# Performance work log

Hardware: AMD Instinct MI355X
Metric: run time of the kernel (lower is better)

## Reference

```python
import jax, jax.numpy as jnp
import numpy as np

N_NODES = 100000
N_EDGES = 1600000
N_GRAPHS = 64


def setup_inputs() -> dict:
    key = jax.random.key(0)
    ks = jax.random.split(key, 12)
    x = jax.random.normal(ks[0], (N_NODES, 3), dtype=jnp.float32)
    edge_index = jax.random.randint(ks[1], (2, N_EDGES), 0, N_NODES)
    edge_attr = jax.random.uniform(ks[2], (N_EDGES,), dtype=jnp.float32)
    batch = jnp.sort(jax.random.randint(ks[3], (N_NODES,), 0, N_GRAPHS))

    def glorot(k, shape):
        lim = float(np.sqrt(6.0 / (shape[0] + shape[1])))
        return jax.random.uniform(k, shape, jnp.float32, -lim, lim)

    W1 = glorot(ks[4], (3, 100));    b1 = jnp.zeros((100,), jnp.float32)
    W2 = glorot(ks[5], (100, 200));  b2 = jnp.zeros((200,), jnp.float32)
    Wl1 = glorot(ks[6], (200, 100)); bl1 = jnp.zeros((100,), jnp.float32)
    Wl2 = glorot(ks[7], (100, 1));   bl2 = jnp.zeros((1,), jnp.float32)
    return {"x": x, "edge_attr": edge_attr, "W1": W1, "b1": b1, "W2": W2,
            "b2": b2, "Wl1": Wl1, "bl1": bl1, "Wl2": Wl2, "bl2": bl2,
            "edge_index": edge_index, "batch": batch}


def gcn_conv(x, edge_index, edge_weight, W, b):
    # PyG GCNConv: linear transform, add self-loops (weight 1), symmetric
    # deg^{-1/2} normalization, scatter-add messages source->target, + bias.
    h = x @ W                                   # [N, out]
    n = h.shape[0]
    loops = jnp.arange(n)
    row = jnp.concatenate([edge_index[0], loops])   # sources
    col = jnp.concatenate([edge_index[1], loops])   # targets
    w = jnp.concatenate([edge_weight, jnp.ones((n,), edge_weight.dtype)])
    deg = jax.ops.segment_sum(w, col, num_segments=n)
    dinv = jnp.where(deg > 0, jax.lax.rsqrt(deg), jnp.zeros_like(deg))
    norm = dinv[row] * w * dinv[col]                # [E+N]
    out = jax.ops.segment_sum(norm[:, None] * h[row], col, num_segments=n)
    return out + b


def reference(x, edge_attr, W1, b1, W2, b2, Wl1, bl1, Wl2, bl2, edge_index, batch):
    h = jax.nn.silu(gcn_conv(x, edge_index, edge_attr, W1, b1))
    h = jax.nn.silu(gcn_conv(h, edge_index, edge_attr, W2, b2))
    # global_mean_pool over graphs in the batch
    sums = jax.ops.segment_sum(h, batch, num_segments=N_GRAPHS)
    counts = jax.ops.segment_sum(jnp.ones((h.shape[0],), h.dtype), batch,
                                 num_segments=N_GRAPHS)
    pooled = sums / jnp.maximum(counts, 1.0)[:, None]   # [G, 200]
    h = jax.nn.silu(pooled @ Wl1 + bl1)
    out = h @ Wl2 + bl2                                  # [G, 1]
    return out.squeeze()
```

## Files before the change

### kernel.cpp

```cpp
#include <hip/hip_runtime.h>

#define NN 100000
#define NE 1600000
#define NG 64
#define CAP 64
#define NPB 80
#define NBUCK 391
#define NBLK 391
#define EPB 4096

__device__ __forceinline__ float silu_f(float x) { return x / (1.0f + __expf(-x)); }

__global__ void k_hist(const int* __restrict__ col, int* __restrict__ hist,
                       float* __restrict__ pooled2) {
  __shared__ int h[NBUCK];
  int tid = threadIdx.x;
  for (int i = tid; i < NBUCK; i += 256) h[i] = 0;
  for (int i = blockIdx.x * 256 + tid; i < NG * 64 * 200; i += NBLK * 256)
    pooled2[i] = 0.0f;
  __syncthreads();
  int s = blockIdx.x * EPB;
  for (int i = 0; i < EPB / 1024; ++i) {
    int e = s + i * 1024 + tid * 4;
    if (e + 3 < NE) {
      int4 c4 = *(const int4*)(col + e);
      atomicAdd(&h[c4.x >> 8], 1);
      atomicAdd(&h[c4.y >> 8], 1);
      atomicAdd(&h[c4.z >> 8], 1);
      atomicAdd(&h[c4.w >> 8], 1);
    } else {
      for (int j = 0; j < 4; ++j) {
        int ee = e + j;
        if (ee < NE) atomicAdd(&h[col[ee] >> 8], 1);
      }
    }
  }
  __syncthreads();
  for (int i = tid; i < NBUCK; i += 256)
    hist[blockIdx.x * NBUCK + i] = h[i];
}

__global__ void k_bscan(const int* __restrict__ hist, int* __restrict__ off_bb,
                        int* __restrict__ tot) {
  __shared__ int m[NBLK][16];
  int tid = threadIdx.x;
  int b0 = blockIdx.x * 16;
  int cb = tid & 15, rr = tid >> 4;
  for (int r = rr; r < NBLK; r += 16) {
    int b = b0 + cb;
    m[r][cb] = (b < NBUCK) ? hist[r * NBUCK + b] : 0;
  }
  __syncthreads();
  if (tid < 16) {
    int run = 0;
    for (int r = 0; r < NBLK; ++r) { int v = m[r][tid]; m[r][tid] = run; run += v; }
    if (b0 + tid < NBUCK) tot[b0 + tid] = run;
  }
  __syncthreads();
  for (int r = rr; r < NBLK; r += 16) {
    int b = b0 + cb;
    if (b < NBUCK) off_bb[r * NBUCK + b] = m[r][cb];
  }
}

__global__ void k_scatter(const int* __restrict__ row, const int* __restrict__ col,
                          const float* __restrict__ ew, const int* __restrict__ off_bb,
                          const int* __restrict__ tot, int* __restrict__ gbase,
                          int2* __restrict__ sorted) {
  __shared__ int pos[NBUCK];
  __shared__ int bs[NBUCK];
  int tid = threadIdx.x;
  if (tid < 64) {
    int lane = tid;
    int loc[7];
    int ssum = 0;
    for (int i = 0; i < 7; ++i) {
      int b = lane * 7 + i;
      loc[i] = ssum;
      ssum += (b < NBUCK) ? tot[b] : 0;
    }
    int inc = ssum;
    for (int d = 1; d < 64; d <<= 1) {
      int t = __shfl_up(inc, d, 64);
      if (lane >= d) inc += t;
    }
    int excl = inc - ssum;
    for (int i = 0; i < 7; ++i) {
      int b = lane * 7 + i;
      if (b < NBUCK) bs[b] = excl + loc[i];
    }
  }
  __syncthreads();
  for (int i = tid; i < NBUCK; i += 256)
    pos[i] = off_bb[blockIdx.x * NBUCK + i] + bs[i];
  if (blockIdx.x == 0) {
    for (int i = tid; i < NBUCK; i += 256) gbase[i] = bs[i];
    if (tid == 0) gbase[NBUCK] = NE;
  }
  __syncthreads();
  int s = blockIdx.x * EPB;
  for (int i = 0; i < EPB / 1024; ++i) {
    int e = s + i * 1024 + tid * 4;
    if (e + 3 < NE) {
      int4 r4 = *(const int4*)(row + e);
      int4 c4 = *(const int4*)(col + e);
      float4 w4 = *(const float4*)(ew + e);
      int p0 = atomicAdd(&pos[c4.x >> 8], 1);
      int p1 = atomicAdd(&pos[c4.y >> 8], 1);
      int p2 = atomicAdd(&pos[c4.z >> 8], 1);
      int p3 = atomicAdd(&pos[c4.w >> 8], 1);
      sorted[p0] = make_int2(r4.x | ((c4.x & 255) << 17), __float_as_int(w4.x));
      sorted[p1] = make_int2(r4.y | ((c4.y & 255) << 17), __float_as_int(w4.y));
      sorted[p2] = make_int2(r4.z | ((c4.z & 255) << 17), __float_as_int(w4.z));
      sorted[p3] = make_int2(r4.w | ((c4.w & 255) << 17), __float_as_int(w4.w));
    } else {
      for (int j = 0; j < 4; ++j) {
        int ee = e + j;
        if (ee < NE) {
          int c = col[ee];
          int p = atomicAdd(&pos[c >> 8], 1);
          sorted[p] = make_int2(row[ee] | ((c & 255) << 17), __float_as_int(ew[ee]));
        }
      }
    }
  }
}

__global__ void k_group(const int* __restrict__ gbase, const int2* __restrict__ sorted,
                        int* __restrict__ cur, int2* __restrict__ buck,
                        float* __restrict__ dinv, const float* __restrict__ x,
                        float* __restrict__ y) {
  __shared__ int cnt[256];
  __shared__ float wsum[256];
  int b = blockIdx.x, tid = threadIdx.x;
  int s = gbase[b], e = gbase[b + 1];
  cnt[tid] = 0; wsum[tid] = 0.0f;
  __syncthreads();
  for (int i = s + tid; i < e; i += 256) {
    int2 pk = sorted[i];
    int node = (pk.x >> 17) & 255;
    int rank = atomicAdd(&cnt[node], 1);
    atomicAdd(&wsum[node], __int_as_float(pk.y));
    if (rank < CAP)
      buck[(((size_t)b * 256 + node) << 6) + rank] = make_int2(pk.x & 0x1FFFF, pk.y);
  }
  __syncthreads();
  int gnode = b * 256 + tid;
  if (gnode < NN) {
    cur[gnode] = cnt[tid];
    float di = rsqrtf(wsum[tid] + 1.0f);
    dinv[gnode] = di;
    y[3 * gnode + 0] = di * x[3 * gnode + 0];
    y[3 * gnode + 1] = di * x[3 * gnode + 1];
    y[3 * gnode + 2] = di * x[3 * gnode + 2];
  }
}

__global__ void k_agg1z(const int* __restrict__ cur, const int2* __restrict__ buck,
                        const float* __restrict__ dinv, const float* __restrict__ y,
                        const float* __restrict__ W1, const float* __restrict__ b1,
                        float* __restrict__ z1p) {
  int wave = threadIdx.x >> 6, lane = threadIdx.x & 63;
  int sub = lane >> 4, rank = lane & 15;
  int cbase = blockIdx.x * 16 + wave * 4;
  int c = cbase + sub;
  int cnt = min(cur[c], CAP);
  float dc = dinv[c];
  float s0 = 0.0f, s1 = 0.0f, s2 = 0.0f;
  for (int p = rank; p < cnt; p += 16) {
    int2 pk = buck[((size_t)c << 6) + p];
    int r = pk.x;
    float ww = __int_as_float(pk.y);
    s0 += ww * y[3 * r + 0];
    s1 += ww * y[3 * r + 1];
    s2 += ww * y[3 * r + 2];
  }
  for (int s = 8; s; s >>= 1) {
    s0 += __shfl_down(s0, s, 16);
    s1 += __shfl_down(s1, s, 16);
    s2 += __shfl_down(s2, s, 16);
  }
  if (rank == 0) {
    s0 = (s0 + y[3 * c + 0]) * dc;
    s1 = (s1 + y[3 * c + 1]) * dc;
    s2 = (s2 + y[3 * c + 2]) * dc;
  }
  float2 w0, w1, w2, bq;
  if (lane < 50) {
    w0 = ((const float2*)(W1))[lane];
    w1 = ((const float2*)(W1 + 100))[lane];
    w2 = ((const float2*)(W1 + 200))[lane];
    bq = ((const float2*)b1)[lane];
  }
#pragma unroll
  for (int n = 0; n < 4; ++n) {
    float t0 = __shfl(s0, n * 16, 64);
    float t1 = __shfl(s1, n * 16, 64);
    float t2 = __shfl(s2, n * 16, 64);
    float dn = __shfl(dc, n * 16, 64);
    if (lane < 50) {
      float2 o;
      o.x = dn * silu_f(bq.x + t0 * w0.x + t1 * w1.x + t2 * w2.x);
      o.y = dn * silu_f(bq.y + t0 * w0.y + t1 * w1.y + t2 * w2.y);
      ((float2*)(z1p + (size_t)(cbase + n) * 100))[lane] = o;
    }
  }
}

__global__ void k_agg2(const float* __restrict__ z1p, const float* __restrict__ dinv,
                       const int* __restrict__ cur, const int2* __restrict__ buck,
                       float* __restrict__ a2) {
  int wave = threadIdx.x >> 6;
  int lane = threadIdx.x & 63;
  int c = blockIdx.x * 4 + wave;
  if (c >= NN) return;
  int grp = lane >> 5;
  int li = lane & 31;
  bool act = li < 25;
  float dc = dinv[c];
  const float4* zv = (const float4*)z1p;
  float4 acc = make_float4(0.f, 0.f, 0.f, 0.f);
  if (grp == 0 && act) {
    float4 v = zv[(size_t)c * 25 + li];
    acc.x = dc * v.x; acc.y = dc * v.y; acc.z = dc * v.z; acc.w = dc * v.w;
  }
  int cnt = min(cur[c], CAP);
  int2 pk = make_int2(0, 0);
  if (lane < cnt) pk = buck[((size_t)c << 6) + lane];
  int p = 0;
#define GATH(off, rv, cv) \
  int rv = __shfl(pk.x, p + (off) + grp, 64); \
  float cv = __int_as_float(__shfl(pk.y, p + (off) + grp, 64)) * dc;
#define ACC(rv, cv) { \
  float4 v = zv[(size_t)rv * 25 + li]; \
  acc.x += cv * v.x; acc.y += cv * v.y; acc.z += cv * v.z; acc.w += cv * v.w; }
  for (; p + 8 <= cnt; p += 8) {
    GATH(0, r0, c0) GATH(2, r1, c1) GATH(4, r2, c2) GATH(6, r3, c3)
    if (act) { ACC(r0, c0) ACC(r1, c1) ACC(r2, c2) ACC(r3, c3) }
  }
  for (; p + 2 <= cnt; p += 2) {
    GATH(0, r0, c0)
    if (act) ACC(r0, c0)
  }
  if (p < cnt) {
    int r0 = __shfl(pk.x, p, 64);
    float c0 = __int_as_float(__shfl(pk.y, p, 64)) * dc;
    if (grp == 0 && act) ACC(r0, c0)
  }
#undef GATH
#undef ACC
  acc.x += __shfl(acc.x, lane + 32, 64);
  acc.y += __shfl(acc.y, lane + 32, 64);
  acc.z += __shfl(acc.z, lane + 32, 64);
  acc.w += __shfl(acc.w, lane + 32, 64);
  if (grp == 0 && act) ((float4*)a2)[(size_t)c * 25 + li] = acc;
}

__global__ void k_h2pool(const float* __restrict__ a2, const float* __restrict__ W2,
                         const float* __restrict__ b2, const int* __restrict__ batch,
                         float* __restrict__ pooled2) {
  __shared__ float zst[100 * 84];
  __shared__ float part[6 * 200];
  __shared__ int bsm[NPB];
  int tid = threadIdx.x;
  int nb = blockIdx.x * NPB;
  int slot = blockIdx.x & 63;
  const float4* a2v = (const float4*)(a2 + (size_t)nb * 100);
  for (int i = tid; i < NPB * 25; i += 256) {
    int n = i / 25, c = i % 25;
    float4 v = a2v[i];
    zst[(4 * c + 0) * 84 + n] = v.x;
    zst[(4 * c + 1) * 84 + n] = v.y;
    zst[(4 * c + 2) * 84 + n] = v.z;
    zst[(4 * c + 3) * 84 + n] = v.w;
  }
  if (tid < NPB) bsm[tid] = batch[nb + tid];
  for (int i = tid; i < 1200; i += 256) part[i] = 0.0f;
  __syncthreads();
  int gmin = bsm[0];
  int ngr = bsm[NPB - 1] - gmin + 1;
  int q = tid % 25;
  int r = tid / 25;
  if (r < 10) {
    int n0 = r * 8;
    float4 acc0[8], acc1[8];
#pragma unroll
    for (int i = 0; i < 8; ++i) {
      acc0[i] = make_float4(0.f, 0.f, 0.f, 0.f);
      acc1[i] = make_float4(0.f, 0.f, 0.f, 0.f);
    }
    const float4* W2v = (const float4*)W2;
#pragma unroll 2
    for (int k = 0; k < 100; ++k) {
      float4 w0 = W2v[k * 50 + 2 * q];
      float4 w1 = W2v[k * 50 + 2 * q + 1];
      float4 za = *(const float4*)&zst[k * 84 + n0];
      float4 zb = *(const float4*)&zst[k * 84 + n0 + 4];
#define FMA8(ai, zv) \
  acc0[ai].x += (zv) * w0.x; acc0[ai].y += (zv) * w0.y; \
  acc0[ai].z += (zv) * w0.z; acc0[ai].w += (zv) * w0.w; \
  acc1[ai].x += (zv) * w1.x; acc1[ai].y += (zv) * w1.y; \
  acc1[ai].z += (zv) * w1.z; acc1[ai].w += (zv) * w1.w;
      FMA8(0, za.x) FMA8(1, za.y) FMA8(2, za.z) FMA8(3, za.w)
      FMA8(4, zb.x) FMA8(5, zb.y) FMA8(6, zb.z) FMA8(7, zb.w)
#undef FMA8
    }
    float4 b0v = ((const float4*)b2)[2 * q];
    float4 b1v = ((const float4*)b2)[2 * q + 1];
    float4 run0 = make_float4(0.f, 0.f, 0.f, 0.f);
    float4 run1 = make_float4(0.f, 0.f, 0.f, 0.f);
    int curg = bsm[n0];
#define FLUSH(gv) { \
  int gl = (gv) - gmin; \
  if (gl < 6) { \
    float* pr = &part[gl * 200 + 8 * q]; \
    atomicAdd(&pr[0], run0.x); atomicAdd(&pr[1], run0.y); \
    atomicAdd(&pr[2], run0.z); atomicAdd(&pr[3], run0.w); \
    atomicAdd(&pr[4], run1.x); atomicAdd(&pr[5], run1.y); \
    atomicAdd(&pr[6], run1.z); atomicAdd(&pr[7], run1.w); \
  } else { \
    float* pr = &pooled2[((size_t)(gv) * 64 + slot) * 200 + 8 * q]; \
    atomicAdd(&pr[0], run0.x); atomicAdd(&pr[1], run0.y); \
    atomicAdd(&pr[2], run0.z); atomicAdd(&pr[3], run0.w); \
    atomicAdd(&pr[4], run1.x); atomicAdd(&pr[5], run1.y); \
    atomicAdd(&pr[6], run1.z); atomicAdd(&pr[7], run1.w); \
  } }
#pragma unroll
    for (int i = 0; i < 8; ++i) {
      float4 s0, s1;
      s0.x = silu_f(acc0[i].x + b0v.x); s0.y = silu_f(acc0[i].y + b0v.y);
      s0.z = silu_f(acc0[i].z + b0v.z); s0.w = silu_f(acc0[i].w + b0v.w);
      s1.x = silu_f(acc1[i].x + b1v.x); s1.y = silu_f(acc1[i].y + b1v.y);
      s1.z = silu_f(acc1[i].z + b1v.z); s1.w = silu_f(acc1[i].w + b1v.w);
      int g = bsm[n0 + i];
      if (g != curg) {
        FLUSH(curg)
        run0 = make_float4(0.f, 0.f, 0.f, 0.f);
        run1 = make_float4(0.f, 0.f, 0.f, 0.f);
        curg = g;
      }
      run0.x += s0.x; run0.y += s0.y; run0.z += s0.z; run0.w += s0.w;
      run1.x += s1.x; run1.y += s1.y; run1.z += s1.z; run1.w += s1.w;
    }
    FLUSH(curg)
#undef FLUSH
  }
  __syncthreads();
  if (tid < 200) {
    int nloop = min(ngr, 6);
    for (int g = 0; g < nloop; ++g)
      pooled2[((size_t)(gmin + g) * 64 + slot) * 200 + tid] = part[g * 200 + tid];
  }
}

__global__ void k_final(const float* __restrict__ pooled2, const int* __restrict__ batch,
                        const float* __restrict__ Wl1, const float* __restrict__ bl1,
                        const float* __restrict__ Wl2, const float* __restrict__ bl2,
                        float* __restrict__ out) {
  __shared__ float pm[200];
  __shared__ float hid[100];
  __shared__ int bounds[2];
  int g = blockIdx.x;
  int j = threadIdx.x;
  if (j < 2) {
    int target = g + j;
    int lo = 0, hi = NN;
    while (lo < hi) {
      int mid = (lo + hi) >> 1;
      if (batch[mid] < target) lo = mid + 1; else hi = mid;
    }
    bounds[j] = lo;
  }
  float acc = 0.0f;
  if (j < 200) {
    const float* base = pooled2 + (size_t)g * 64 * 200 + j;
    for (int s = 0; s < 64; ++s) acc += base[s * 200];
  }
  __syncthreads();
  int cntg = bounds[1] - bounds[0];
  float inv = 1.0f / (float)((cntg > 0) ? cntg : 1);
  if (j < 200) pm[j] = acc * inv;
  __syncthreads();
  if (j < 100) {
    float a = bl1[j];
    for (int k = 0; k < 200; ++k) a += pm[k] * Wl1[k * 100 + j];
    a = silu_f(a);
    hid[j] = a * Wl2[j];
  }
  __syncthreads();
  if (j == 0) {
    float sum = bl2[0];
    for (int k = 0; k < 100; ++k) sum += hid[k];
    out[g] = sum;
  }
}

extern "C" void kernel_launch(void* const* d_in, const int* in_sizes, int n_in,
                              void* d_out, int out_size, void* d_ws, size_t ws_size,
                              hipStream_t stream) {
  const float* x   = (const float*)d_in[0];
  const float* ew  = (const float*)d_in[1];
  const float* W1  = (const float*)d_in[2];
  const float* b1  = (const float*)d_in[3];
  const float* W2  = (const float*)d_in[4];
  const float* b2  = (const float*)d_in[5];
  const float* Wl1 = (const float*)d_in[6];
  const float* bl1 = (const float*)d_in[7];
  const float* Wl2 = (const float*)d_in[8];
  const float* bl2 = (const float*)d_in[9];
  const int* ei    = (const int*)d_in[10];
  const int* batch = (const int*)d_in[11];
  const int* rowp = ei;
  const int* colp = ei + NE;
  float* out = (float*)d_out;

  char* w = (char*)d_ws;
  size_t o = 0;
  auto alloc = [&](size_t bytes) {
    char* p = w + o;
    o = (o + bytes + 255) & ~(size_t)255;
    return p;
  };
  int*   cur     = (int*)alloc((size_t)NN * 4);
  float* dinv    = (float*)alloc((size_t)NN * 4);
  float* y       = (float*)alloc((size_t)NN * 3 * 4);
  float* pooled2 = (float*)alloc((size_t)NG * 64 * 200 * 4);
  float* z1p     = (float*)alloc((size_t)NN * 100 * 4);
  float* a2      = (float*)alloc((size_t)NN * 100 * 4);
  int2*  buck    = (int2*)alloc((size_t)NN * CAP * 8);
  int2*  sorted  = (int2*)alloc((size_t)NE * 8);
  int*   hist    = (int*)alloc((size_t)NBLK * NBUCK * 4);
  int*   off_bb  = (int*)alloc((size_t)NBLK * NBUCK * 4);
  int*   tot     = (int*)alloc((size_t)NBUCK * 4);
  int*   gbase   = (int*)alloc((size_t)(NBUCK + 1) * 4);

  k_hist<<<NBLK, 256, 0, stream>>>(colp, hist, pooled2);
  k_bscan<<<(NBUCK + 15) / 16, 256, 0, stream>>>(hist, off_bb, tot);
  k_scatter<<<NBLK, 256, 0, stream>>>(rowp, colp, ew, off_bb, tot, gbase, sorted);
  k_group<<<NBUCK, 256, 0, stream>>>(gbase, sorted, cur, buck, dinv, x, y);
  k_agg1z<<<NN / 16, 256, 0, stream>>>(cur, buck, dinv, y, W1, b1, z1p);
  k_agg2<<<(NN + 3) / 4, 256, 0, stream>>>(z1p, dinv, cur, buck, a2);
  k_h2pool<<<NN / NPB, 256, 0, stream>>>(a2, W2, b2, batch, pooled2);
  k_final<<<NG, 256, 0, stream>>>(pooled2, batch, Wl1, bl1, Wl2, bl2, out);
}
```

Baseline: 354.8 us.

## Fuse edge-sorting kernels into one cooperative kernel and pad node features to float4

Merges the histogram, bucket scan, scatter and group kernels into a single cooperative kernel that uses grid-wide syncs between phases, removing three kernel launches and their inter-kernel gaps. It also stores the scaled input features as float4 so each gathered neighbour needs one vector load instead of three scalar loads. In exchange, the fused kernel uses more shared memory (the 391x16 scan tile plus buffers), which may lower occupancy, and it depends on all 391 blocks being co-resident for the grid sync. The padded feature array also takes more memory.

```diff
diff --git a/kernel.cpp b/kernel.cpp
--- a/kernel.cpp
+++ b/kernel.cpp
@@ -1,4 +1,7 @@
 #include <hip/hip_runtime.h>
+#include <hip/hip_cooperative_groups.h>
+
+namespace cg = cooperative_groups;
 
 #define NN 100000
 #define NE 1600000
@@ -11,15 +14,25 @@
 
 __device__ __forceinline__ float silu_f(float x) { return x / (1.0f + __expf(-x)); }
 
-__global__ void k_hist(const int* __restrict__ col, int* __restrict__ hist,
-                       float* __restrict__ pooled2) {
+__global__ void k_build(const int* __restrict__ row, const int* __restrict__ col,
+                        const float* __restrict__ ew, const float* __restrict__ x,
+                        int* __restrict__ hist, int* __restrict__ off_bb,
+                        int* __restrict__ tot, int* __restrict__ gbase,
+                        int2* __restrict__ sorted, int* __restrict__ cur,
+                        int2* __restrict__ buck, float* __restrict__ dinv,
+                        float4* __restrict__ y4, float* __restrict__ pooled2) {
+  cg::grid_group grid = cg::this_grid();
   __shared__ int h[NBUCK];
+  __shared__ int bs[NBUCK];
+  __shared__ int m[NBLK][16];
+  __shared__ float wsum[256];
   int tid = threadIdx.x;
+  int blk = blockIdx.x;
+
   for (int i = tid; i < NBUCK; i += 256) h[i] = 0;
-  for (int i = blockIdx.x * 256 + tid; i < NG * 64 * 200; i += NBLK * 256)
-    pooled2[i] = 0.0f;
-  __syncthreads();
-  int s = blockIdx.x * EPB;
+  for (int i = blk * 256 + tid; i < NG * 64 * 200; i += NBLK * 256) pooled2[i] = 0.0f;
+  __syncthreads();
+  int s = blk * EPB;
   for (int i = 0; i < EPB / 1024; ++i) {
     int e = s + i * 1024 + tid * 4;
     if (e + 3 < NE) {
@@ -36,40 +49,30 @@
     }
   }
   __syncthreads();
-  for (int i = tid; i < NBUCK; i += 256)
-    hist[blockIdx.x * NBUCK + i] = h[i];
-}
-
-__global__ void k_bscan(const int* __restrict__ hist, int* __restrict__ off_bb,
-                        int* __restrict__ tot) {
-  __shared__ int m[NBLK][16];
-  int tid = threadIdx.x;
-  int b0 = blockIdx.x * 16;
-  int cb = tid & 15, rr = tid >> 4;
-  for (int r = rr; r < NBLK; r += 16) {
-    int b = b0 + cb;
-    m[r][cb] = (b < NBUCK) ? hist[r * NBUCK + b] : 0;
-  }
-  __syncthreads();
-  if (tid < 16) {
-    int run = 0;
-    for (int r = 0; r < NBLK; ++r) { int v = m[r][tid]; m[r][tid] = run; run += v; }
-    if (b0 + tid < NBUCK) tot[b0 + tid] = run;
-  }
-  __syncthreads();
-  for (int r = rr; r < NBLK; r += 16) {
-    int b = b0 + cb;
-    if (b < NBUCK) off_bb[r * NBUCK + b] = m[r][cb];
-  }
-}
-
-__global__ void k_scatter(const int* __restrict__ row, const int* __restrict__ col,
-                          const float* __restrict__ ew, const int* __restrict__ off_bb,
-                          const int* __restrict__ tot, int* __restrict__ gbase,
-                          int2* __restrict__ sorted) {
-  __shared__ int pos[NBUCK];
-  __shared__ int bs[NBUCK];
-  int tid = threadIdx.x;
+  for (int i = tid; i < NBUCK; i += 256) hist[blk * NBUCK + i] = h[i];
+  grid.sync();
+
+  if (blk < (NBUCK + 15) / 16) {
+    int b0 = blk * 16;
+    int cb = tid & 15, rr = tid >> 4;
+    for (int r = rr; r < NBLK; r += 16) {
+      int b = b0 + cb;
+      m[r][cb] = (b < NBUCK) ? hist[r * NBUCK + b] : 0;
+    }
+    __syncthreads();
+    if (tid < 16) {
+      int run = 0;
+      for (int r = 0; r < NBLK; ++r) { int v = m[r][tid]; m[r][tid] = run; run += v; }
+      if (b0 + tid < NBUCK) tot[b0 + tid] = run;
+    }
+    __syncthreads();
+    for (int r = rr; r < NBLK; r += 16) {
+      int b = b0 + cb;
+      if (b < NBUCK) off_bb[r * NBUCK + b] = m[r][cb];
+    }
+  }
+  grid.sync();
+
   if (tid < 64) {
     int lane = tid;
     int loc[7];
@@ -92,23 +95,22 @@
   }
   __syncthreads();
   for (int i = tid; i < NBUCK; i += 256)
-    pos[i] = off_bb[blockIdx.x * NBUCK + i] + bs[i];
-  if (blockIdx.x == 0) {
+    h[i] = off_bb[blk * NBUCK + i] + bs[i];
+  if (blk == 0) {
     for (int i = tid; i < NBUCK; i += 256) gbase[i] = bs[i];
     if (tid == 0) gbase[NBUCK] = NE;
   }
   __syncthreads();
-  int s = blockIdx.x * EPB;
   for (int i = 0; i < EPB / 1024; ++i) {
     int e = s + i * 1024 + tid * 4;
     if (e + 3 < NE) {
       int4 r4 = *(const int4*)(row + e);
       int4 c4 = *(const int4*)(col + e);
       float4 w4 = *(const float4*)(ew + e);
-      int p0 = atomicAdd(&pos[c4.x >> 8], 1);
-      int p1 = atomicAdd(&pos[c4.y >> 8], 1);
-      int p2 = atomicAdd(&pos[c4.z >> 8], 1);
-      int p3 = atomicAdd(&pos[c4.w >> 8], 1);
+      int p0 = atomicAdd(&h[c4.x >> 8], 1);
+      int p1 = atomicAdd(&h[c4.y >> 8], 1);
+      int p2 = atomicAdd(&h[c4.z >> 8], 1);
+      int p3 = atomicAdd(&h[c4.w >> 8], 1);
       sorted[p0] = make_int2(r4.x | ((c4.x & 255) << 17), __float_as_int(w4.x));
       sorted[p1] = make_int2(r4.y | ((c4.y & 255) << 17), __float_as_int(w4.y));
       sorted[p2] = make_int2(r4.z | ((c4.z & 255) << 17), __float_as_int(w4.z));
@@ -118,46 +120,41 @@
         int ee = e + j;
         if (ee < NE) {
           int c = col[ee];
-          int p = atomicAdd(&pos[c >> 8], 1);
+          int p = atomicAdd(&h[c >> 8], 1);
           sorted[p] = make_int2(row[ee] | ((c & 255) << 17), __float_as_int(ew[ee]));
         }
       }
     }
   }
-}
-
-__global__ void k_group(const int* __restrict__ gbase, const int2* __restrict__ sorted,
-                        int* __restrict__ cur, int2* __restrict__ buck,
-                        float* __restrict__ dinv, const float* __restrict__ x,
-                        float* __restrict__ y) {
-  __shared__ int cnt[256];
-  __shared__ float wsum[256];
-  int b = blockIdx.x, tid = threadIdx.x;
-  int s = gbase[b], e = gbase[b + 1];
-  cnt[tid] = 0; wsum[tid] = 0.0f;
-  __syncthreads();
-  for (int i = s + tid; i < e; i += 256) {
-    int2 pk = sorted[i];
-    int node = (pk.x >> 17) & 255;
-    int rank = atomicAdd(&cnt[node], 1);
-    atomicAdd(&wsum[node], __int_as_float(pk.y));
-    if (rank < CAP)
-      buck[(((size_t)b * 256 + node) << 6) + rank] = make_int2(pk.x & 0x1FFFF, pk.y);
-  }
-  __syncthreads();
-  int gnode = b * 256 + tid;
-  if (gnode < NN) {
-    cur[gnode] = cnt[tid];
-    float di = rsqrtf(wsum[tid] + 1.0f);
-    dinv[gnode] = di;
-    y[3 * gnode + 0] = di * x[3 * gnode + 0];
-    y[3 * gnode + 1] = di * x[3 * gnode + 1];
-    y[3 * gnode + 2] = di * x[3 * gnode + 2];
+  grid.sync();
+
+  {
+    int b = blk;
+    int s4 = gbase[b], e4 = gbase[b + 1];
+    h[tid] = 0; wsum[tid] = 0.0f;
+    __syncthreads();
+    for (int i = s4 + tid; i < e4; i += 256) {
+      int2 pk = sorted[i];
+      int node = (pk.x >> 17) & 255;
+      int rank = atomicAdd(&h[node], 1);
+      atomicAdd(&wsum[node], __int_as_float(pk.y));
+      if (rank < CAP)
+        buck[(((size_t)b * 256 + node) << 6) + rank] = make_int2(pk.x & 0x1FFFF, pk.y);
+    }
+    __syncthreads();
+    int gnode = b * 256 + tid;
+    if (gnode < NN) {
+      cur[gnode] = h[tid];
+      float di = rsqrtf(wsum[tid] + 1.0f);
+      dinv[gnode] = di;
+      y4[gnode] = make_float4(di * x[3 * gnode + 0], di * x[3 * gnode + 1],
+                              di * x[3 * gnode + 2], 0.0f);
+    }
   }
 }
 
 __global__ void k_agg1z(const int* __restrict__ cur, const int2* __restrict__ buck,
-                        const float* __restrict__ dinv, const float* __restrict__ y,
+                        const float* __restrict__ dinv, const float4* __restrict__ y4,
                         const float* __restrict__ W1, const float* __restrict__ b1,
                         float* __restrict__ z1p) {
   int wave = threadIdx.x >> 6, lane = threadIdx.x & 63;
@@ -169,11 +166,11 @@
   float s0 = 0.0f, s1 = 0.0f, s2 = 0.0f;
   for (int p = rank; p < cnt; p += 16) {
     int2 pk = buck[((size_t)c << 6) + p];
-    int r = pk.x;
     float ww = __int_as_float(pk.y);
-    s0 += ww * y[3 * r + 0];
-    s1 += ww * y[3 * r + 1];
-    s2 += ww * y[3 * r + 2];
+    float4 v = y4[pk.x];
+    s0 += ww * v.x;
+    s1 += ww * v.y;
+    s2 += ww * v.z;
   }
   for (int s = 8; s; s >>= 1) {
     s0 += __shfl_down(s0, s, 16);
@@ -181,9 +178,10 @@
     s2 += __shfl_down(s2, s, 16);
   }
   if (rank == 0) {
-    s0 = (s0 + y[3 * c + 0]) * dc;
-    s1 = (s1 + y[3 * c + 1]) * dc;
-    s2 = (s2 + y[3 * c + 2]) * dc;
+    float4 vc = y4[c];
+    s0 = (s0 + vc.x) * dc;
+    s1 = (s1 + vc.y) * dc;
+    s2 = (s2 + vc.z) * dc;
   }
   float2 w0, w1, w2, bq;
   if (lane < 50) {
@@ -421,24 +419,26 @@
     o = (o + bytes + 255) & ~(size_t)255;
     return p;
   };
-  int*   cur     = (int*)alloc((size_t)NN * 4);
-  float* dinv    = (float*)alloc((size_t)NN * 4);
-  float* y       = (float*)alloc((size_t)NN * 3 * 4);
-  float* pooled2 = (float*)alloc((size_t)NG * 64 * 200 * 4);
-  float* z1p     = (float*)alloc((size_t)NN * 100 * 4);
-  float* a2      = (float*)alloc((size_t)NN * 100 * 4);
-  int2*  buck    = (int2*)alloc((size_t)NN * CAP * 8);
-  int2*  sorted  = (int2*)alloc((size_t)NE * 8);
-  int*   hist    = (int*)alloc((size_t)NBLK * NBUCK * 4);
-  int*   off_bb  = (int*)alloc((size_t)NBLK * NBUCK * 4);
-  int*   tot     = (int*)alloc((size_t)NBUCK * 4);
-  int*   gbase   = (int*)alloc((size_t)(NBUCK + 1) * 4);
-
-  k_hist<<<NBLK, 256, 0, stream>>>(colp, hist, pooled2);
-  k_bscan<<<(NBUCK + 15) / 16, 256, 0, stream>>>(hist, off_bb, tot);
-  k_scatter<<<NBLK, 256, 0, stream>>>(rowp, colp, ew, off_bb, tot, gbase, sorted);
-  k_group<<<NBUCK, 256, 0, stream>>>(gbase, sorted, cur, buck, dinv, x, y);
-  k_agg1z<<<NN / 16, 256, 0, stream>>>(cur, buck, dinv, y, W1, b1, z1p);
+  int*    cur     = (int*)alloc((size_t)NN * 4);
+  float*  dinv    = (float*)alloc((size_t)NN * 4);
+  float4* y4      = (float4*)alloc((size_t)NN * 16);
+  float*  pooled2 = (float*)alloc((size_t)NG * 64 * 200 * 4);
+  float*  z1p     = (float*)alloc((size_t)NN * 100 * 4);
+  float*  a2      = (float*)alloc((size_t)NN * 100 * 4);
+  int2*   buck    = (int2*)alloc((size_t)NN * CAP * 8);
+  int2*   sorted  = (int2*)alloc((size_t)NE * 8);
+  int*    hist    = (int*)alloc((size_t)NBLK * NBUCK * 4);
+  int*    off_bb  = (int*)alloc((size_t)NBLK * NBUCK * 4);
+  int*    tot     = (int*)alloc((size_t)NBUCK * 4);
+  int*    gbase   = (int*)alloc((size_t)(NBUCK + 1) * 4);
+
+  void* args[] = {(void*)&rowp, (void*)&colp, (void*)&ew, (void*)&x,
+                  (void*)&hist, (void*)&off_bb, (void*)&tot, (void*)&gbase,
+                  (void*)&sorted, (void*)&cur, (void*)&buck, (void*)&dinv,
+                  (void*)&y4, (void*)&pooled2};
+  hipLaunchCooperativeKernel((void*)k_build, dim3(NBLK), dim3(256), args, 0, stream);
+
+  k_agg1z<<<NN / 16, 256, 0, stream>>>(cur, buck, dinv, y4, W1, b1, z1p);
   k_agg2<<<(NN + 3) / 4, 256, 0, stream>>>(z1p, dinv, cur, buck, a2);
   k_h2pool<<<NN / NPB, 256, 0, stream>>>(a2, W2, b2, batch, pooled2);
   k_final<<<NG, 256, 0, stream>>>(pooled2, batch, Wl1, bl1, Wl2, bl2, out);
```

Result: slower. 504.9 us (+42.3%).
